# Optimization experiments

Measured on AMD Instinct MI355X. Metric: run time of the kernel, lower is better.

The kernel has to match this reference:

```python
import jax, jax.numpy as jnp
import numpy as np

N, L, D = 4, 4096, 1024
H = 16
HD = D // H          # 64
MLP = 4 * D          # 4096
EPS = 1e-5

def log_g(x):
    # torch: where(x>=0, log(relu(x)+0.5), -softplus(-x))
    return jnp.where(x >= 0.0, jnp.log(jax.nn.relu(x) + 0.5), -jax.nn.softplus(-x))

def parallel_scan_log(log_coeffs, log_values):
    # log_coeffs: (B, L, C); log_values: (B, L+1, C)
    a_star = jnp.pad(jnp.cumsum(log_coeffs, axis=1), ((0, 0), (1, 0), (0, 0)))
    log_h = jax.lax.cumlogsumexp(log_values - a_star, axis=1)
    return jnp.exp(a_star[:, 1:] + log_h[:, 1:])

def layer_norm(x, gamma, beta):
    mu = jnp.mean(x, axis=-1, keepdims=True)
    var = jnp.var(x, axis=-1, keepdims=True)
    return (x - mu) * jax.lax.rsqrt(var + EPS) * gamma + beta

def setup_inputs() -> dict:
    key = jax.random.key(0)
    ks = jax.random.split(key, 12)
    s = 0.02
    return {
        "x": jax.random.normal(ks[0], (N, L, D), jnp.float32),
        "h_0": jax.random.normal(ks[1], (N, 1, D), jnp.float32),
        "w_in": jax.random.normal(ks[2], (D, D), jnp.float32) * s,
        "b_in": jnp.zeros((D,), jnp.float32),
        "wz": jax.random.normal(ks[3], (HD, HD), jnp.float32) * s,
        "bz": jnp.zeros((HD,), jnp.float32),
        "wh": jax.random.normal(ks[4], (HD, HD), jnp.float32) * s,
        "bh": jnp.zeros((HD,), jnp.float32),
        "w_out": jax.random.normal(ks[5], (D, D), jnp.float32) * s,
        "b_out": jnp.zeros((D,), jnp.float32),
        "ln1_g": jnp.ones((D,), jnp.float32),
        "ln1_b": jnp.zeros((D,), jnp.float32),
        "ln2_g": jnp.ones((D,), jnp.float32),
        "ln2_b": jnp.zeros((D,), jnp.float32),
        "mw1": jax.random.normal(ks[6], (D, MLP), jnp.float32) * s,
        "mb1": jnp.zeros((MLP,), jnp.float32),
        "mw2": jax.random.normal(ks[7], (MLP, MLP), jnp.float32) * s,
        "mb2": jnp.zeros((MLP,), jnp.float32),
        "mw3": jax.random.normal(ks[8], (MLP, D), jnp.float32) * s,
        "mb3": jnp.zeros((D,), jnp.float32),
    }

def reference(x, h_0, w_in, b_in, wz, bz, wh, bh, w_out, b_out,
              ln1_g, ln1_b, ln2_g, ln2_b, mw1, mb1, mw2, mb2, mw3, mb3):
    n, l, d = x.shape
    rnn_input = layer_norm(x, ln1_g, ln1_b)
    pi = rnn_input @ w_in + b_in                                 # (N,L,D)
    pi = pi.reshape(n, l, H, HD).transpose(0, 2, 1, 3).reshape(n * H, l, HD)
    h0 = h_0.reshape(n, 1, H, HD).transpose(0, 2, 1, 3).reshape(n * H, 1, HD)
    # minGRU in log-space
    k = pi @ wz + bz
    log_z = -jax.nn.softplus(-k)
    log_coeffs = -jax.nn.softplus(k)
    log_h0 = log_g(h0)
    log_th = log_g(pi @ wh + bh)
    h = parallel_scan_log(log_coeffs, jnp.concatenate([log_h0, log_z + log_th], axis=1))
    rnn_states = h.reshape(n, H, l, HD).transpose(0, 2, 1, 3).reshape(n, l, d)
    x = x + (rnn_states @ w_out + b_out)
    mlp_in = layer_norm(x, ln2_g, ln2_b)
    y = jax.nn.silu(mlp_in @ mw1 + mb1)
    y = jax.nn.silu(y @ mw2 + mb2)
    y = y @ mw3 + mb3
    return (x + y, rnn_states)
```

## Files before the change

kernel.cpp:

```cpp
#include <hip/hip_runtime.h>
#include <hip/hip_bf16.h>

typedef __attribute__((ext_vector_type(8))) short short8;
typedef __attribute__((ext_vector_type(4))) short short4v;
typedef __attribute__((ext_vector_type(4))) float f32x4;
using bf16 = __hip_bfloat16;

#define DEV static __device__ __forceinline__

DEV float bf2f(bf16 v) { return __bfloat162float(v); }
DEV bf16 f2bf(float v) { return __float2bfloat16(v); }
DEV float s2f(short s) {
  union { unsigned u; float f; } v;
  v.u = ((unsigned)(unsigned short)s) << 16;
  return v.f;
}
DEV short f2s(float v) {
  bf16 b = __float2bfloat16(v);
  return *(short*)&b;
}

DEV void gld_lds16(const void* g, void* l) {
  __builtin_amdgcn_global_load_lds(
      (const __attribute__((address_space(1))) void*)g,
      (__attribute__((address_space(3))) void*)l, 16, 0, 0);
}

__global__ __launch_bounds__(256)
void wconv_kernel(const float* __restrict__ w, bf16* __restrict__ wT, int K, int N) {
  __shared__ float tile[32][33];
  const int kt = blockIdx.x * 32, nt = blockIdx.y * 32;
  const int tx = threadIdx.x & 31, ty = threadIdx.x >> 5;
#pragma unroll
  for (int i = 0; i < 32; i += 8)
    tile[ty + i][tx] = w[(size_t)(kt + ty + i) * N + nt + tx];
  __syncthreads();
#pragma unroll
  for (int i = 0; i < 32; i += 8)
    wT[(size_t)(nt + ty + i) * K + kt + tx] = f2bf(tile[tx][ty + i]);
}

__global__ __launch_bounds__(256)
void ln_kernel(const float* __restrict__ x, const float* __restrict__ g,
               const float* __restrict__ b, bf16* __restrict__ out) {
  const int row = blockIdx.x;
  const int t = threadIdx.x;
  const float4 v = ((const float4*)(x + (size_t)row * 1024))[t];
  float s = v.x + v.y + v.z + v.w;
  float ss = v.x * v.x + v.y * v.y + v.z * v.z + v.w * v.w;
#pragma unroll
  for (int off = 32; off > 0; off >>= 1) {
    s += __shfl_down(s, off);
    ss += __shfl_down(ss, off);
  }
  __shared__ float red[8];
  if ((t & 63) == 0) { red[(t >> 6) * 2] = s; red[(t >> 6) * 2 + 1] = ss; }
  __syncthreads();
  s = red[0] + red[2] + red[4] + red[6];
  ss = red[1] + red[3] + red[5] + red[7];
  const float mu = s * (1.f / 1024.f);
  const float rstd = rsqrtf(ss * (1.f / 1024.f) - mu * mu + 1e-5f);
  const float4 g4 = ((const float4*)g)[t];
  const float4 b4 = ((const float4*)b)[t];
  struct alignas(8) B4 { bf16 v[4]; } o;
  o.v[0] = f2bf((v.x - mu) * rstd * g4.x + b4.x);
  o.v[1] = f2bf((v.y - mu) * rstd * g4.y + b4.y);
  o.v[2] = f2bf((v.z - mu) * rstd * g4.z + b4.z);
  o.v[3] = f2bf((v.w - mu) * rstd * g4.w + b4.w);
  *(B4*)(out + (size_t)row * 1024 + t * 4) = o;
}

template <int EPI>
__global__ __launch_bounds__(256, 2)
void gemm128(const bf16* __restrict__ A, const bf16* __restrict__ BT,
             const float* __restrict__ bias, const float* __restrict__ res,
             void* __restrict__ C, int M, int N, int K) {
  __shared__ short As[128 * 64];
  __shared__ short Bs[128 * 64];
  const int tid = threadIdx.x;
  const int l = tid & 63;
  const int w = tid >> 6;
  const int wr = w >> 1, wc = w & 1;

  const int nbn = N >> 7;
  const int nwg = gridDim.x;
  const int bid = blockIdx.x;
  const int q = nwg >> 3, r = nwg & 7;
  const int xcd = bid & 7, lin = bid >> 3;
  const int wg = (xcd < r ? xcd * (q + 1) : r * (q + 1) + (xcd - r) * q) + lin;
  const int bm = wg / nbn, bn = wg % nbn;

  const bf16* Ab = A + (size_t)bm * 128 * K;
  const bf16* Bb = BT + (size_t)bn * 128 * K;

  f32x4 acc[4][4];
#pragma unroll
  for (int i = 0; i < 4; ++i)
#pragma unroll
    for (int j = 0; j < 4; ++j) acc[i][j] = (f32x4){0.f, 0.f, 0.f, 0.f};

  const int srow = l >> 3;
  const int scol = (((l & 7) ^ (l >> 3)) << 3);

  for (int k0 = 0; k0 < K; k0 += 64) {
    __syncthreads();
#pragma unroll
    for (int p = 0; p < 4; ++p) {
      const int rowA = p * 32 + w * 8 + srow;
      gld_lds16(Ab + (size_t)rowA * K + k0 + scol, As + (p * 32 + w * 8) * 64);
      gld_lds16(Bb + (size_t)rowA * K + k0 + scol, Bs + (p * 32 + w * 8) * 64);
    }
    __syncthreads();
    const int xr = (l & 7) << 3;
#pragma unroll
    for (int kk = 0; kk < 2; ++kk) {
      short8 fa[4], fb[4];
#pragma unroll
      for (int m = 0; m < 4; ++m)
        fa[m] = *(const short8*)&As[(wr * 64 + m * 16 + (l & 15)) * 64 +
                                    ((kk * 32 + (l >> 4) * 8) ^ xr)];
#pragma unroll
      for (int n = 0; n < 4; ++n)
        fb[n] = *(const short8*)&Bs[(wc * 64 + n * 16 + (l & 15)) * 64 +
                                    ((kk * 32 + (l >> 4) * 8) ^ xr)];
#pragma unroll
      for (int m = 0; m < 4; ++m)
#pragma unroll
        for (int n = 0; n < 4; ++n)
          acc[m][n] = __builtin_amdgcn_mfma_f32_16x16x32_bf16(fa[m], fb[n], acc[m][n], 0, 0, 0);
    }
  }

  const int lc = l & 15;
  const int lr = (l >> 4) * 4;
  float bv4[2];
#pragma unroll
  for (int n = 0; n < 2; ++n) bv4[n] = 0.f;
#pragma unroll
  for (int m = 0; m < 4; ++m) {
    const int row = bm * 128 + wr * 64 + m * 16 + lr;
#pragma unroll
    for (int r2 = 0; r2 < 4; ++r2) {
      const size_t rowoff = (size_t)(row + r2) * N;
#pragma unroll
      for (int n = 0; n < 4; ++n) {
        const int col = bn * 128 + wc * 64 + n * 16 + lc;
        float v = acc[m][n][r2] + bias[col];
        const size_t off = rowoff + col;
        if constexpr (EPI == 1) v = v / (1.f + __expf(-v));
        if constexpr (EPI == 2) {
          ((float*)C)[off] = res[off] + v;
        } else {
          ((bf16*)C)[off] = f2bf(v);
        }
      }
    }
  }
  (void)M; (void)bv4;
}

template <int EPI>
__global__ __launch_bounds__(512, 2)
void gemm256(const bf16* __restrict__ A, const bf16* __restrict__ BT,
             const float* __restrict__ bias, const float* __restrict__ res,
             void* __restrict__ C, int M, int N, int K) {
  __shared__ alignas(16) short As[2][256 * 64];
  __shared__ alignas(16) short Bs[2][256 * 64];
  const int tid = threadIdx.x;
  const int l = tid & 63;
  const int w = tid >> 6;
  const int wr = w >> 2;
  const int wc = w & 3;

  const int nbn = N >> 8;
  const int nwg = gridDim.x;
  const int bid = blockIdx.x;
  const int q = nwg >> 3, r = nwg & 7;
  const int xcd = bid & 7, lin = bid >> 3;
  const int wg = (xcd < r ? xcd * (q + 1) : r * (q + 1) + (xcd - r) * q) + lin;
  const int bm = wg / nbn, bn = wg % nbn;

  const bf16* Ab = A + (size_t)bm * 256 * K;
  const bf16* Bb = BT + (size_t)bn * 256 * K;

  const int gcol = ((l & 7) ^ (l >> 3)) << 3;
  const int fr = l & 15;
  const int kq = (l >> 4) << 3;
  const int xr = (l & 7) << 3;
  const int k0s = kq ^ xr;
  const int k1s = (32 + kq) ^ xr;

  const bf16* Abl = Ab + (size_t)(w * 16 + (l >> 3)) * K + gcol;
  const bf16* Bbl = Bb + (size_t)(w * 16 + (l >> 3)) * K + gcol;

  f32x4 acc[8][4];
#pragma unroll
  for (int i = 0; i < 8; ++i)
#pragma unroll
    for (int j = 0; j < 4; ++j) acc[i][j] = (f32x4){0.f, 0.f, 0.f, 0.f};

  short8 fa[2][2];
  short8 fb[4][2];

#define BARX() __builtin_amdgcn_s_barrier()
#define SBAR0() __builtin_amdgcn_sched_barrier(0)

#define STAGE_A(BUF, HALF, KT)                                                     \
  do {                                                                             \
    gld_lds16(Abl + (size_t)((HALF) * 128) * K + (size_t)(KT) * 64,                \
              &As[BUF][((HALF) * 128 + w * 16) * 64]);                             \
    gld_lds16(Abl + (size_t)((HALF) * 128 + 8) * K + (size_t)(KT) * 64,            \
              &As[BUF][((HALF) * 128 + w * 16 + 8) * 64]);                         \
  } while (0)

#define STAGE_B(BUF, HALF, KT)                                                     \
  do {                                                                             \
    gld_lds16(Bbl + (size_t)((HALF) * 128) * K + (size_t)(KT) * 64,                \
              &Bs[BUF][((HALF) * 128 + w * 16) * 64]);                             \
    gld_lds16(Bbl + (size_t)((HALF) * 128 + 8) * K + (size_t)(KT) * 64,            \
              &Bs[BUF][((HALF) * 128 + w * 16 + 8) * 64]);                         \
  } while (0)

#define RD_FA(BUF, Q)                                                                    \
  do {                                                                                  \
    fa[0][0] = *(const short8*)&As[BUF][(wr * 128 + (Q) * 32 + fr) * 64 + k0s];         \
    fa[0][1] = *(const short8*)&As[BUF][(wr * 128 + (Q) * 32 + fr) * 64 + k1s];         \
    fa[1][0] = *(const short8*)&As[BUF][(wr * 128 + (Q) * 32 + 16 + fr) * 64 + k0s];    \
    fa[1][1] = *(const short8*)&As[BUF][(wr * 128 + (Q) * 32 + 16 + fr) * 64 + k1s];    \
  } while (0)

#define RD_FB(BUF)                                                                      \
  do {                                                                                 \
    _Pragma("unroll") for (int n_ = 0; n_ < 4; ++n_) {                                 \
      fb[n_][0] = *(const short8*)&Bs[BUF][(wc * 64 + n_ * 16 + fr) * 64 + k0s];       \
      fb[n_][1] = *(const short8*)&Bs[BUF][(wc * 64 + n_ * 16 + fr) * 64 + k1s];       \
    }                                                                                  \
  } while (0)

#define MMA_Q(Q)                                                                        \
  do {                                                                                 \
    __builtin_amdgcn_s_setprio(1);                                                     \
    _Pragma("unroll") for (int n_ = 0; n_ < 4; ++n_) {                                 \
      acc[2 * (Q)][n_] = __builtin_amdgcn_mfma_f32_16x16x32_bf16(                      \
          fa[0][0], fb[n_][0], acc[2 * (Q)][n_], 0, 0, 0);                             \
      acc[2 * (Q) + 1][n_] = __builtin_amdgcn_mfma_f32_16x16x32_bf16(                  \
          fa[1][0], fb[n_][0], acc[2 * (Q) + 1][n_], 0, 0, 0);                         \
    }                                                                                  \
    _Pragma("unroll") for (int n_ = 0; n_ < 4; ++n_) {                                 \
      acc[2 * (Q)][n_] = __builtin_amdgcn_mfma_f32_16x16x32_bf16(                      \
          fa[0][1], fb[n_][1], acc[2 * (Q)][n_], 0, 0, 0);                             \
      acc[2 * (Q) + 1][n_] = __builtin_amdgcn_mfma_f32_16x16x32_bf16(                  \
          fa[1][1], fb[n_][1], acc[2 * (Q) + 1][n_], 0, 0, 0);                         \
    }                                                                                  \
    __builtin_amdgcn_s_setprio(0);                                                     \
  } while (0)

#define LGKM0() do { asm volatile("s_waitcnt lgkmcnt(0)"); SBAR0(); } while (0)

#define TILE(BUF, T, HASA, HASB)                                                       \
  do {                                                                                 \
                                                                               \
    LGKM0();                                                                           \
    MMA_Q(0);                                                                          \
    if (HASA) { STAGE_A((BUF) ^ 1, 0, (T) + 1); STAGE_A((BUF) ^ 1, 1, (T) + 1); }      \
    RD_FA(BUF, 1);                                                                     \
    SBAR0(); BARX();                                                                   \
                                                                               \
    LGKM0();                                                                           \
    MMA_Q(1);                                                                          \
    RD_FA(BUF, 2);                                                                     \
    SBAR0(); BARX();                                                                   \
                                                                               \
    LGKM0();                                                                           \
    MMA_Q(2);                                                                          \
    if (HASB) STAGE_B(BUF, 0, (T) + 2);                                                \
    if (HASA) {                                                                        \
      if (HASB) asm volatile("s_waitcnt vmcnt(2)" ::: "memory");                       \
      else      asm volatile("s_waitcnt vmcnt(0)" ::: "memory");                       \
    }                                                                                  \
    RD_FA(BUF, 3);                                                                     \
    SBAR0(); BARX();                                                                   \
                                                                               \
    LGKM0();                                                                           \
    MMA_Q(3);                                                                          \
    if (HASB) STAGE_B(BUF, 1, (T) + 2);                                                \
    if (HASA) {                                                                        \
      RD_FB((BUF) ^ 1);                                                                \
      RD_FA((BUF) ^ 1, 0);                                                             \
      SBAR0(); BARX();                                                                 \
    }                                                                                  \
  } while (0)

  STAGE_A(0, 0, 0); STAGE_A(0, 1, 0);
  STAGE_B(0, 0, 0); STAGE_B(0, 1, 0);
  STAGE_B(1, 0, 1); STAGE_B(1, 1, 1);
  asm volatile("s_waitcnt vmcnt(4)" ::: "memory");
  BARX();
  RD_FB(0);
  RD_FA(0, 0);

  const int NT = K >> 6;
  const int NI = NT >> 1;
#pragma unroll 1
  for (int i = 0; i < NI; ++i) {
    const int t0 = 2 * i;
    const bool b0 = (t0 + 2) < NT;
    const bool b1 = (t0 + 3) < NT;
    TILE(0, t0, true, b0);
    TILE(1, t0 + 1, b0, b1);
  }

#undef BARX
#undef SBAR0
#undef STAGE_A
#undef STAGE_B
#undef RD_FA
#undef RD_FB
#undef MMA_Q
#undef LGKM0
#undef TILE

  const int lc = l & 15;
  const int lr = (l >> 4) * 4;
#pragma unroll
  for (int m = 0; m < 8; ++m) {
    const int row = bm * 256 + wr * 128 + m * 16 + lr;
#pragma unroll
    for (int r2 = 0; r2 < 4; ++r2) {
      const size_t rowoff = (size_t)(row + r2) * N;
#pragma unroll
      for (int n = 0; n < 4; ++n) {
        const int col = bn * 256 + wc * 64 + n * 16 + lc;
        float v = acc[m][n][r2] + bias[col];
        const size_t off = rowoff + col;
        if constexpr (EPI == 1) v = v / (1.f + __expf(-v));
        if constexpr (EPI == 2) {
          ((float*)C)[off] = res[off] + v;
        } else {
          ((bf16*)C)[off] = f2bf(v);
        }
      }
    }
  }
  (void)M;
}

__global__ __launch_bounds__(256)
void heads_kernel(const bf16* __restrict__ piB,
                  const float* __restrict__ wz, const float* __restrict__ bz,
                  const float* __restrict__ wh, const float* __restrict__ bh,
                  bf16* __restrict__ aB, bf16* __restrict__ bB,
                  float* __restrict__ cA, float* __restrict__ cB) {
  __shared__ float wzs[4096], whs[4096], pis[4096];
  __shared__ float segA[4][64], segB[4][64];
  const int h = blockIdx.y;
  const int t0 = blockIdx.x * 64;
  const int tid = threadIdx.x;
#pragma unroll
  for (int i = tid; i < 4096; i += 256) {
    wzs[i] = wz[i];
    whs[i] = wh[i];
  }
#pragma unroll
  for (int rr = 0; rr < 4; ++rr) {
    const int v = tid + rr * 256;
    const int row = v >> 4, c4 = (v & 15) * 4;
    short4v p4 = *(const short4v*)(piB + (size_t)(t0 + row) * 1024 + h * 64 + c4);
    pis[row * 64 + c4 + 0] = s2f(p4[0]);
    pis[row * 64 + c4 + 1] = s2f(p4[1]);
    pis[row * 64 + c4 + 2] = s2f(p4[2]);
    pis[row * 64 + c4 + 3] = s2f(p4[3]);
  }
  __syncthreads();
  const int hd = tid & 63;
  const int tb = (tid >> 6) * 16;
  float accK[16], accT[16];
  const float bzv = bz[hd], bhv = bh[hd];
#pragma unroll
  for (int i = 0; i < 16; ++i) { accK[i] = bzv; accT[i] = bhv; }
  for (int j = 0; j < 64; ++j) {
    const float wzv = wzs[j * 64 + hd];
    const float whv = whs[j * 64 + hd];
#pragma unroll
    for (int i = 0; i < 16; ++i) {
      const float p = pis[(tb + i) * 64 + j];
      accK[i] = fmaf(p, wzv, accK[i]);
      accT[i] = fmaf(p, whv, accT[i]);
    }
  }
  float As = 1.f, Bs = 0.f;
#pragma unroll
  for (int i = 0; i < 16; ++i) {
    const float k = accK[i], th = accT[i];
    const float sig = 1.f / (1.f + __expf(-k));
    const float a = 1.f - sig;
    const float gg = th >= 0.f ? th + 0.5f : 1.f / (1.f + __expf(-th));
    const float bb = sig * gg;
    Bs = fmaf(a, Bs, bb);
    As *= a;
    const size_t idx = (size_t)(t0 + tb + i) * 1024 + h * 64 + hd;
    aB[idx] = f2bf(a);
    bB[idx] = f2bf(bb);
  }
  segA[tid >> 6][hd] = As;
  segB[tid >> 6][hd] = Bs;
  __syncthreads();
  if (tid < 64) {
    float A = segA[0][tid], B = segB[0][tid];
#pragma unroll
    for (int s = 1; s < 4; ++s) {
      B = fmaf(segA[s][tid], B, segB[s][tid]);
      A *= segA[s][tid];
    }
    const int n = t0 >> 12;
    const int chunk = (t0 >> 6) & 63;
    const size_t o = ((size_t)(n * 64 + chunk)) * 1024 + h * 64 + tid;
    cA[o] = A;
    cB[o] = B;
  }
}

__global__ __launch_bounds__(256)
void scan_phase2(const float* __restrict__ h0,
                 const float* __restrict__ cA, const float* __restrict__ cB,
                 float* __restrict__ hst) {
  const int idx = blockIdx.x * 256 + threadIdx.x;
  const int c = idx & 1023;
  const int n = idx >> 10;
  float hv = h0[(size_t)n * 1024 + c];
  hv = hv >= 0.f ? hv + 0.5f : 1.f / (1.f + __expf(-hv));
  for (int ch = 0; ch < 64; ++ch) {
    const size_t o = ((size_t)(n * 64 + ch)) * 1024 + c;
    hst[o] = hv;
    hv = fmaf(cA[o], hv, cB[o]);
  }
}

__global__ __launch_bounds__(128)
void scan_phase3(const bf16* __restrict__ aB, const bf16* __restrict__ bB,
                 const float* __restrict__ hst,
                 float* __restrict__ rnn, bf16* __restrict__ rnnB) {
  const int idx = blockIdx.x * 128 + threadIdx.x;
  const int c8 = idx & 127;
  const int chunk = (idx >> 7) & 63;
  const int n = idx >> 13;
  const int c0 = c8 * 8;
  float hv[8];
  const float4* hsrc = (const float4*)(hst + ((size_t)(n * 64 + chunk)) * 1024 + c0);
  float4 ha = hsrc[0], hb = hsrc[1];
  hv[0] = ha.x; hv[1] = ha.y; hv[2] = ha.z; hv[3] = ha.w;
  hv[4] = hb.x; hv[5] = hb.y; hv[6] = hb.z; hv[7] = hb.w;
  size_t base = ((size_t)(n * 4096 + chunk * 64)) * 1024 + c0;
#pragma unroll 4
  for (int s = 0; s < 64; ++s) {
    const short8 a8 = *(const short8*)(aB + base);
    const short8 b8 = *(const short8*)(bB + base);
    short8 ob;
    float4 o0, o1;
#pragma unroll
    for (int j = 0; j < 8; ++j) {
      hv[j] = fmaf(s2f(a8[j]), hv[j], s2f(b8[j]));
      ob[j] = f2s(hv[j]);
    }
    o0.x = hv[0]; o0.y = hv[1]; o0.z = hv[2]; o0.w = hv[3];
    o1.x = hv[4]; o1.y = hv[5]; o1.z = hv[6]; o1.w = hv[7];
    ((float4*)(rnn + base))[0] = o0;
    ((float4*)(rnn + base))[1] = o1;
    *(short8*)(rnnB + base) = ob;
    base += 1024;
  }
}

extern "C" void kernel_launch(void* const* d_in, const int* in_sizes, int n_in,
                              void* d_out, int out_size, void* d_ws, size_t ws_size,
                              hipStream_t stream) {
  const float* x    = (const float*)d_in[0];
  const float* h0   = (const float*)d_in[1];
  const float* w_in = (const float*)d_in[2];
  const float* b_in = (const float*)d_in[3];
  const float* wz   = (const float*)d_in[4];
  const float* bz   = (const float*)d_in[5];
  const float* wh   = (const float*)d_in[6];
  const float* bh   = (const float*)d_in[7];
  const float* w_out= (const float*)d_in[8];
  const float* b_out= (const float*)d_in[9];
  const float* ln1g = (const float*)d_in[10];
  const float* ln1b = (const float*)d_in[11];
  const float* ln2g = (const float*)d_in[12];
  const float* ln2b = (const float*)d_in[13];
  const float* mw1  = (const float*)d_in[14];
  const float* mb1  = (const float*)d_in[15];
  const float* mw2  = (const float*)d_in[16];
  const float* mb2  = (const float*)d_in[17];
  const float* mw3  = (const float*)d_in[18];
  const float* mb3  = (const float*)d_in[19];
  (void)in_sizes; (void)n_in; (void)out_size;

  float* out0 = (float*)d_out;
  float* out1 = (float*)d_out + (size_t)16384 * 1024;

  char* ws = (char*)d_ws;
  size_t o = 0;
  auto take = [&](size_t bytes) { char* p = ws + o; o += (bytes + 255) & ~(size_t)255; return p; };
  bf16* w_inT = (bf16*)take((size_t)1024 * 1024 * 2);
  bf16* w_outT= (bf16*)take((size_t)1024 * 1024 * 2);
  bf16* mw1T  = (bf16*)take((size_t)4096 * 1024 * 2);
  bf16* mw2T  = (bf16*)take((size_t)4096 * 4096 * 2);
  bf16* mw3T  = (bf16*)take((size_t)4096 * 1024 * 2);
  bf16* lnxB  = (bf16*)take((size_t)16384 * 1024 * 2);
  bf16* piB   = (bf16*)take((size_t)16384 * 1024 * 2);
  bf16* aB    = (bf16*)take((size_t)16384 * 1024 * 2);
  bf16* bB    = (bf16*)take((size_t)16384 * 1024 * 2);
  float* cA   = (float*)take((size_t)4 * 64 * 1024 * 4);
  float* cB   = (float*)take((size_t)4 * 64 * 1024 * 4);
  float* hst  = (float*)take((size_t)4 * 64 * 1024 * 4);
  if (o > ws_size) return;

  wconv_kernel<<<dim3(32, 32), 256, 0, stream>>>(w_in, w_inT, 1024, 1024);
  wconv_kernel<<<dim3(32, 32), 256, 0, stream>>>(w_out, w_outT, 1024, 1024);
  wconv_kernel<<<dim3(32, 128), 256, 0, stream>>>(mw1, mw1T, 1024, 4096);
  wconv_kernel<<<dim3(128, 128), 256, 0, stream>>>(mw2, mw2T, 4096, 4096);
  wconv_kernel<<<dim3(128, 32), 256, 0, stream>>>(mw3, mw3T, 4096, 1024);

  ln_kernel<<<16384, 256, 0, stream>>>(x, ln1g, ln1b, lnxB);
  gemm256<0><<<256, 512, 0, stream>>>(lnxB, w_inT, b_in, nullptr, piB, 16384, 1024, 1024);

  heads_kernel<<<dim3(256, 16), 256, 0, stream>>>(piB, wz, bz, wh, bh, aB, bB, cA, cB);
  scan_phase2<<<16, 256, 0, stream>>>(h0, cA, cB, hst);
  scan_phase3<<<256, 128, 0, stream>>>(aB, bB, hst, out1, lnxB );

  gemm256<2><<<256, 512, 0, stream>>>(lnxB, w_outT, b_out, x, out0, 16384, 1024, 1024);

  ln_kernel<<<16384, 256, 0, stream>>>(out0, ln2g, ln2b, lnxB );
  bf16* t1 = aB;
  bf16* t2 = bB;
  for (int mc = 0; mc < 4; ++mc) {
    const bf16* a3 = lnxB + (size_t)mc * 4096 * 1024;
    gemm256<1><<<256, 512, 0, stream>>>(a3, mw1T, mb1, nullptr, t1, 4096, 4096, 1024);
    gemm256<1><<<256, 512, 0, stream>>>(t1, mw2T, mb2, nullptr, t2, 4096, 4096, 4096);
    float* oc = out0 + (size_t)mc * 4096 * 1024;
    gemm128<2><<<256, 256, 0, stream>>>(t2, mw3T, mb3, oc, oc, 4096, 1024, 4096);
  }
}
```

Baseline: 1.294 ms.

## Triple-buffer A tiles in gemm256 to prefetch two K-steps ahead

Grows the A shared-memory staging from two to three buffers and rewrites the main loop as a rotating-buffer pipeline. A tiles are now prefetched two K-tiles ahead instead of one, with vmcnt waits retuned to match. The aim is to hide more global-load latency behind MFMA work. LDS use rises from 128KB to 160KB per block, which can cut occupancy below the requested two blocks per CU. Runtime buffer indices also replace the compile-time ones.

```diff
diff --git a/kernel.cpp b/kernel.cpp
--- a/kernel.cpp
+++ b/kernel.cpp
@@ -133,9 +133,6 @@
 
   const int lc = l & 15;
   const int lr = (l >> 4) * 4;
-  float bv4[2];
-#pragma unroll
-  for (int n = 0; n < 2; ++n) bv4[n] = 0.f;
 #pragma unroll
   for (int m = 0; m < 4; ++m) {
     const int row = bm * 128 + wr * 64 + m * 16 + lr;
@@ -156,7 +153,7 @@
       }
     }
   }
-  (void)M; (void)bv4;
+  (void)M;
 }
 
 template <int EPI>
@@ -164,7 +161,7 @@
 void gemm256(const bf16* __restrict__ A, const bf16* __restrict__ BT,
              const float* __restrict__ bias, const float* __restrict__ res,
              void* __restrict__ C, int M, int N, int K) {
-  __shared__ alignas(16) short As[2][256 * 64];
+  __shared__ alignas(16) short As[3][256 * 64];
   __shared__ alignas(16) short Bs[2][256 * 64];
   const int tid = threadIdx.x;
   const int l = tid & 63;
@@ -205,19 +202,19 @@
 #define BARX() __builtin_amdgcn_s_barrier()
 #define SBAR0() __builtin_amdgcn_sched_barrier(0)
 
-#define STAGE_A(BUF, HALF, KT)                                                     \
+#define STAGE_A(BUF, HALF, P)                                                      \
   do {                                                                             \
-    gld_lds16(Abl + (size_t)((HALF) * 128) * K + (size_t)(KT) * 64,                \
+    gld_lds16((P) + (size_t)((HALF) * 128) * K,                                    \
               &As[BUF][((HALF) * 128 + w * 16) * 64]);                             \
-    gld_lds16(Abl + (size_t)((HALF) * 128 + 8) * K + (size_t)(KT) * 64,            \
+    gld_lds16((P) + (size_t)((HALF) * 128 + 8) * K,                                \
               &As[BUF][((HALF) * 128 + w * 16 + 8) * 64]);                         \
   } while (0)
 
-#define STAGE_B(BUF, HALF, KT)                                                     \
+#define STAGE_B(BUF, HALF, P)                                                      \
   do {                                                                             \
-    gld_lds16(Bbl + (size_t)((HALF) * 128) * K + (size_t)(KT) * 64,                \
+    gld_lds16((P) + (size_t)((HALF) * 128) * K,                                    \
               &Bs[BUF][((HALF) * 128 + w * 16) * 64]);                             \
-    gld_lds16(Bbl + (size_t)((HALF) * 128 + 8) * K + (size_t)(KT) * 64,            \
+    gld_lds16((P) + (size_t)((HALF) * 128 + 8) * K,                                \
               &Bs[BUF][((HALF) * 128 + w * 16 + 8) * 64]);                         \
   } while (0)
 
@@ -257,57 +254,55 @@
 
 #define LGKM0() do { asm volatile("s_waitcnt lgkmcnt(0)"); SBAR0(); } while (0)
 
-#define TILE(BUF, T, HASA, HASB)                                                       \
-  do {                                                                                 \
-                                                                               \
-    LGKM0();                                                                           \
-    MMA_Q(0);                                                                          \
-    if (HASA) { STAGE_A((BUF) ^ 1, 0, (T) + 1); STAGE_A((BUF) ^ 1, 1, (T) + 1); }      \
-    RD_FA(BUF, 1);                                                                     \
-    SBAR0(); BARX();                                                                   \
-                                                                               \
-    LGKM0();                                                                           \
-    MMA_Q(1);                                                                          \
-    RD_FA(BUF, 2);                                                                     \
-    SBAR0(); BARX();                                                                   \
-                                                                               \
-    LGKM0();                                                                           \
-    MMA_Q(2);                                                                          \
-    if (HASB) STAGE_B(BUF, 0, (T) + 2);                                                \
-    if (HASA) {                                                                        \
-      if (HASB) asm volatile("s_waitcnt vmcnt(2)" ::: "memory");                       \
-      else      asm volatile("s_waitcnt vmcnt(0)" ::: "memory");                       \
-    }                                                                                  \
-    RD_FA(BUF, 3);                                                                     \
-    SBAR0(); BARX();                                                                   \
-                                                                               \
-    LGKM0();                                                                           \
-    MMA_Q(3);                                                                          \
-    if (HASB) STAGE_B(BUF, 1, (T) + 2);                                                \
-    if (HASA) {                                                                        \
-      RD_FB((BUF) ^ 1);                                                                \
-      RD_FA((BUF) ^ 1, 0);                                                             \
-      SBAR0(); BARX();                                                                 \
-    }                                                                                  \
-  } while (0)
-
-  STAGE_A(0, 0, 0); STAGE_A(0, 1, 0);
-  STAGE_B(0, 0, 0); STAGE_B(0, 1, 0);
-  STAGE_B(1, 0, 1); STAGE_B(1, 1, 1);
-  asm volatile("s_waitcnt vmcnt(4)" ::: "memory");
+  STAGE_A(0, 0, Abl); STAGE_A(0, 1, Abl);
+  STAGE_B(0, 0, Bbl); STAGE_B(0, 1, Bbl);
+  STAGE_A(1, 0, Abl + 64); STAGE_A(1, 1, Abl + 64);
+  STAGE_B(1, 0, Bbl + 64); STAGE_B(1, 1, Bbl + 64);
+  asm volatile("s_waitcnt vmcnt(8)" ::: "memory");
   BARX();
   RD_FB(0);
   RD_FA(0, 0);
 
   const int NT = K >> 6;
-  const int NI = NT >> 1;
+  int a0 = 0, a1 = 1, a2 = 2;
+  int bB_ = 0;
+  const bf16* pfA = Abl + 2 * 64;
+  const bf16* pfB = Bbl + 2 * 64;
 #pragma unroll 1
-  for (int i = 0; i < NI; ++i) {
-    const int t0 = 2 * i;
-    const bool b0 = (t0 + 2) < NT;
-    const bool b1 = (t0 + 3) < NT;
-    TILE(0, t0, true, b0);
-    TILE(1, t0 + 1, b0, b1);
+  for (int t = 0; t < NT; ++t) {
+    const bool pf = (t + 2) < NT;
+    const bool nx = (t + 1) < NT;
+    LGKM0();
+    MMA_Q(0);
+    if (pf) STAGE_A(a2, 0, pfA);
+    RD_FA(a0, 1);
+    SBAR0(); BARX();
+    LGKM0();
+    MMA_Q(1);
+    if (pf) STAGE_A(a2, 1, pfA);
+    RD_FA(a0, 2);
+    SBAR0(); BARX();
+    LGKM0();
+    MMA_Q(2);
+    if (pf) {
+      STAGE_B(bB_, 0, pfB);
+      asm volatile("s_waitcnt vmcnt(6)" ::: "memory");
+    } else {
+      asm volatile("s_waitcnt vmcnt(0)" ::: "memory");
+    }
+    RD_FA(a0, 3);
+    SBAR0(); BARX();
+    LGKM0();
+    MMA_Q(3);
+    if (pf) STAGE_B(bB_, 1, pfB);
+    if (nx) {
+      RD_FB(bB_ ^ 1);
+      RD_FA(a1, 0);
+      SBAR0(); BARX();
+    }
+    const int tmp = a0; a0 = a1; a1 = a2; a2 = tmp;
+    bB_ ^= 1;
+    pfA += 64; pfB += 64;
   }
 
 #undef BARX
@@ -318,7 +313,6 @@
 #undef RD_FB
 #undef MMA_Q
 #undef LGKM0
-#undef TILE
 
   const int lc = l & 15;
   const int lr = (l >> 4) * 4;
```

New measurement: 1.476 ms. 14.1% more time.
